# Kernel tuning notes

Measured on AMD Instinct MI355X. Metric: run time of the kernel, lower is better.

Reference implementation:

```python
import jax, jax.numpy as jnp
import numpy as np
import math

B, C, L_SEQ, PRED = 32, 21, 512, 96
D, H, DFF, NLAYERS = 512, 8, 2048, 3
E = D // H
PATCH_LEN, STRIDE, PAD = 16, 8, 8
PATCH_NUM = (L_SEQ - PATCH_LEN) // STRIDE + 2  # 64
MA = 25          # moving-average kernel of series_decomp
FACTOR = 1
TOP_K = int(FACTOR * math.log(PATCH_NUM))  # top-k delays in AutoCorrelation


def _pos_embedding(max_len, d_model):
    pos = np.arange(max_len, dtype=np.float32)[:, None]
    div = np.exp(np.arange(0, d_model, 2, dtype=np.float32) * -(math.log(10000.0) / d_model))
    pe = np.zeros((max_len, d_model), np.float32)
    pe[:, 0::2] = np.sin(pos * div)
    pe[:, 1::2] = np.cos(pos * div)
    return jnp.asarray(pe)

POS_EMB = _pos_embedding(PATCH_NUM, D)


def setup_inputs():
    key = jax.random.key(0)
    ks = iter(jax.random.split(key, 48))
    g = lambda shape, s=0.02: jax.random.normal(next(ks), shape, jnp.float32) * s
    inp = {"x_enc": jax.random.normal(next(ks), (B, L_SEQ, C), jnp.float32)}
    inp["w_val"] = g((PATCH_LEN, D))  # PatchEmbedding value_embedding (no bias)
    for tag in ("ac", "sa"):
        for nm in ("Wq", "Wk", "Wv", "Wo"):
            inp[nm + "_" + tag] = g((NLAYERS, D, D))
        for nm in ("bq", "bk", "bv", "bo"):
            inp[nm + "_" + tag] = g((NLAYERS, D))
    inp["Wf"] = g((NLAYERS, 2 * D, D))
    inp["bf"] = g((NLAYERS, D))
    inp["W1"] = g((NLAYERS, D, DFF))   # conv1 (1x1, no bias)
    inp["W2"] = g((NLAYERS, DFF, D))   # conv2 (1x1, no bias)
    inp["bn_g"] = jnp.ones((D,), jnp.float32)
    inp["bn_b"] = jnp.zeros((D,), jnp.float32)
    inp["W_head"] = g((D * PATCH_NUM, PRED))
    inp["b_head"] = g((PRED,))
    return inp


def _proj_heads(x, W, b):
    N, L, _ = x.shape
    return (x @ W + b).reshape(N, L, H, E)


def _auto_corr(x, Wq, bq, Wk, bk, Wv, bv, Wo, bo):
    # AutoCorrelation (training-mode time_delay_agg): FFT correlation + top-k roll aggregation
    N, L, _ = x.shape
    q = _proj_heads(x, Wq, bq)
    k = _proj_heads(x, Wk, bk)
    v = _proj_heads(x, Wv, bv)
    qf = jnp.fft.rfft(q.transpose(0, 2, 3, 1), axis=-1)   # [N,H,E,Lf]
    kf = jnp.fft.rfft(k.transpose(0, 2, 3, 1), axis=-1)
    corr = jnp.fft.irfft(qf * jnp.conj(kf), n=L, axis=-1)  # [N,H,E,L]
    vals = v.transpose(0, 2, 3, 1)                          # [N,H,E,L]
    mean_corr = corr.mean(axis=(1, 2))                      # [N,L]
    _, top_idx = jax.lax.top_k(mean_corr.mean(axis=0), TOP_K)  # delays shared across batch
    w = jax.nn.softmax(mean_corr[:, top_idx], axis=-1)      # [N,TOP_K]
    rolled = jax.vmap(lambda s: jnp.roll(vals, -s, axis=-1))(top_idx)  # [K,N,H,E,L]
    agg = jnp.einsum('knhel,nk->nhel', rolled, w)
    return agg.transpose(0, 3, 1, 2).reshape(N, L, D) @ Wo + bo


def _full_attn(x, Wq, bq, Wk, bk, Wv, bv, Wo, bo):
    N, L, _ = x.shape
    q = _proj_heads(x, Wq, bq)
    k = _proj_heads(x, Wk, bk)
    v = _proj_heads(x, Wv, bv)
    scores = jnp.einsum('blhe,bshe->bhls', q, k) / math.sqrt(E)
    out = jnp.einsum('bhls,bshe->blhe', jax.nn.softmax(scores, axis=-1), v)
    return out.reshape(N, L, D) @ Wo + bo


def _decomp(x):
    # series_decomp: residual after edge-replicated moving average (returns seasonal part)
    half = (MA - 1) // 2
    xp = jnp.concatenate([jnp.repeat(x[:, :1], half, axis=1), x,
                          jnp.repeat(x[:, -1:], half, axis=1)], axis=1)
    cs = jnp.cumsum(xp, axis=1)
    cs = jnp.concatenate([jnp.zeros_like(cs[:, :1]), cs], axis=1)
    mean = (cs[:, MA:] - cs[:, :-MA]) / MA
    return x - mean


def _forward(x_enc, w_val, Wq_ac, bq_ac, Wk_ac, bk_ac, Wv_ac, bv_ac, Wo_ac, bo_ac,
             Wq_sa, bq_sa, Wk_sa, bk_sa, Wv_sa, bv_sa, Wo_sa, bo_sa,
             Wf, bf, W1, W2, bn_g, bn_b, W_head, b_head):
    # instance normalization over time
    means = x_enc.mean(axis=1, keepdims=True)                 # [B,1,C]
    xc = x_enc - means
    stdev = jnp.sqrt(xc.var(axis=1, keepdims=True) + 1e-5)    # [B,1,C]
    xn = xc / stdev
    # patch embedding (channel independent): replication-pad end, unfold, linear + pos emb
    xp = xn.transpose(0, 2, 1)                                # [B,C,L]
    xp = jnp.concatenate([xp, jnp.repeat(xp[..., -1:], PAD, axis=-1)], axis=-1)
    idx = jnp.arange(PATCH_NUM)[:, None] * STRIDE + jnp.arange(PATCH_LEN)[None, :]
    patches = xp[..., idx]                                    # [B,C,P,patch_len]
    x = patches.reshape(B * C, PATCH_NUM, PATCH_LEN) @ w_val + POS_EMB  # [B*C,P,D]
    # hybrid encoder layers
    for l in range(NLAYERS):
        a = _auto_corr(x, Wq_ac[l], bq_ac[l], Wk_ac[l], bk_ac[l], Wv_ac[l], bv_ac[l], Wo_ac[l], bo_ac[l])
        s = _full_attn(x, Wq_sa[l], bq_sa[l], Wk_sa[l], bk_sa[l], Wv_sa[l], bv_sa[l], Wo_sa[l], bo_sa[l])
        fused = jnp.concatenate([a, s], axis=-1) @ Wf[l] + bf[l]
        x = _decomp(x + fused)
        y = jax.nn.relu(x @ W1[l]) @ W2[l]                    # 1x1 convs == pointwise linears
        x = _decomp(x + y)
    # final BatchNorm1d over d_model channels (batch statistics, affine)
    mu = x.mean(axis=(0, 1))
    var = x.var(axis=(0, 1))
    x = (x - mu) / jnp.sqrt(var + 1e-5) * bn_g + bn_b
    # head: [B*C,P,D] -> [B,C,D,P] -> flat (d-major) -> pred_len
    enc = x.reshape(B, C, PATCH_NUM, D).transpose(0, 1, 3, 2).reshape(B, C, D * PATCH_NUM)
    dec = (enc @ W_head + b_head).transpose(0, 2, 1)          # [B,PRED,C]
    return dec * stdev[:, 0][:, None, :] + means[:, 0][:, None, :]


def reference(x_enc, w_val, Wq_ac, bq_ac, Wk_ac, bk_ac, Wv_ac, bv_ac, Wo_ac, bo_ac,
              Wq_sa, bq_sa, Wk_sa, bk_sa, Wv_sa, bv_sa, Wo_sa, bo_sa,
              Wf, bf, W1, W2, bn_g, bn_b, W_head, b_head):
    return _forward(x_enc, w_val, Wq_ac, bq_ac, Wk_ac, bk_ac, Wv_ac, bv_ac, Wo_ac, bo_ac,
                    Wq_sa, bq_sa, Wk_sa, bk_sa, Wv_sa, bv_sa, Wo_sa, bo_sa,
                    Wf, bf, W1, W2, bn_g, bn_b, W_head, b_head)
```

## Files before the change

kernel.cpp:

```cpp
#include <hip/hip_runtime.h>
#include <math.h>


typedef unsigned short u16;
typedef short s16x8 __attribute__((ext_vector_type(8)));
typedef u16 u16x8 __attribute__((ext_vector_type(8)));
typedef float f32x4 __attribute__((ext_vector_type(4)));

#define MROWS 43008
#define NSEQ  672

__device__ __forceinline__ float bf2f(u16 b) {
  union { unsigned u; float f; } v; v.u = ((unsigned)b) << 16; return v.f;
}
__device__ __forceinline__ u16 f2bf(float f) {
  union { float f; unsigned u; } v; v.f = f;
  unsigned r = v.u + 0x7FFFu + ((v.u >> 16) & 1u);
  return (u16)(r >> 16);
}

__device__ __forceinline__ void gload16(const u16* g, u16* l) {
  __builtin_amdgcn_global_load_lds(
      (const __attribute__((address_space(1))) unsigned int*)g,
      (__attribute__((address_space(3))) unsigned int*)l, 16, 0, 0);
}

__global__ __launch_bounds__(256) void zero_out_kernel(float* __restrict__ o, int n) {
  int i = blockIdx.x * 256 + threadIdx.x;
  if (i < n) o[i] = 0.f;
}

__global__ __launch_bounds__(256) void transpose_cvt_b(
    const float* __restrict__ W, u16* __restrict__ Wt, int K, int N,
    long long sW, long long sT) {
  __shared__ float t[32][33];
  int z = blockIdx.z;
  W += (size_t)z * sW;
  Wt += (size_t)z * sT;
  int k0 = blockIdx.x * 32, n0 = blockIdx.y * 32;
  int tx = threadIdx.x, ty = threadIdx.y;
#pragma unroll
  for (int i = 0; i < 32; i += 8)
    t[ty + i][tx] = W[(size_t)(k0 + ty + i) * N + n0 + tx];
  __syncthreads();
#pragma unroll
  for (int i = 0; i < 32; i += 8)
    Wt[(size_t)(n0 + ty + i) * K + k0 + tx] = f2bf(t[tx][ty + i]);
}

__global__ __launch_bounds__(256) void transpose_cvt_sa(
    const float* __restrict__ Wq_sa, const float* __restrict__ Wk_sa,
    const float* __restrict__ Wv_sa, u16* __restrict__ dst) {
  __shared__ float t[32][33];
  int z = blockIdx.z;
  int l = z / 3, wi = z % 3;
  const float* srcs[3] = {Wq_sa, Wk_sa, Wv_sa};
  const float* W = srcs[wi] + (size_t)l * 262144;
  u16* out = dst + ((size_t)l * 3 + wi) * 262144;
  int k0 = blockIdx.x * 32, n0 = blockIdx.y * 32;
  int tx = threadIdx.x, ty = threadIdx.y;
#pragma unroll
  for (int i = 0; i < 32; i += 8)
    t[ty + i][tx] = W[(size_t)(k0 + ty + i) * 512 + n0 + tx];
  __syncthreads();
#pragma unroll
  for (int i = 0; i < 32; i += 8)
    out[(size_t)(n0 + ty + i) * 512 + k0 + tx] = f2bf(t[tx][ty + i]);
}

__global__ __launch_bounds__(256) void cvt_bf16_fifteen(
    const float* __restrict__ Wo_ac, const float* __restrict__ Wo_sa,
    const float* __restrict__ Wv_ac, const float* __restrict__ Wq_ac,
    const float* __restrict__ Wk_ac, u16* __restrict__ dst) {
  int z = blockIdx.z;
  int l = z / 5, s = z % 5;
  const float* bases[5] = {Wo_ac, Wo_sa, Wv_ac, Wq_ac, Wk_ac};
  const float* src = bases[s] + (size_t)l * 262144;
  u16* out = dst + ((size_t)l * 5 + s) * 262144;
  int i = blockIdx.x * 256 + threadIdx.x;
  if (i < 262144) out[i] = f2bf(src[i]);
}

__global__ __launch_bounds__(512) void boa_eff_kernel(
    const float* __restrict__ Wo_ac, const float* __restrict__ bo_ac,
    const float* __restrict__ bv_ac, float* __restrict__ out) {
  int l = blockIdx.x;
  int i = threadIdx.x;
  const float* Wo = Wo_ac + (size_t)l * 262144;
  float s = bo_ac[l * 512 + i];
  for (int k = 0; k < 512; k++) s += bv_ac[l * 512 + k] * Wo[(size_t)k * 512 + i];
  out[l * 512 + i] = s;
}

__global__ __launch_bounds__(512) void bias_combine(
    const float* __restrict__ WfW, const float* __restrict__ bfW,
    const float* __restrict__ boa_eff, const float* __restrict__ bo_sa,
    float* __restrict__ out) {
  int l = blockIdx.x;
  const float* Wf = WfW + (size_t)l * 524288;
  int n = threadIdx.x;
  float s = bfW[l * 512 + n];
  for (int i = 0; i < 512; i++) s += boa_eff[l * 512 + i] * Wf[(size_t)i * 512 + n];
  for (int i = 0; i < 512; i++) s += bo_sa[l * 512 + i] * Wf[(size_t)(512 + i) * 512 + n];
  out[l * 512 + n] = s;
}

__global__ __launch_bounds__(512, 4) void gemm128x256_p3(
    const u16* __restrict__ A1, const u16* __restrict__ A2, int lda, int ksplit,
    const u16* __restrict__ Bt, int ldb,
    const float* __restrict__ b0, const float* __restrict__ b1,
    const float* __restrict__ b2,
    u16* __restrict__ C, int ldc, int K, int relu, int nb) {
  __shared__ u16 smA[2][128 * 32];
  __shared__ u16 smB[2][256 * 32];
  int g = blockIdx.x;
  if ((gridDim.x & 7) == 0) g = (g & 7) * (gridDim.x >> 3) + (g >> 3);
  int m0 = (g / nb) * 128, n0 = (g % nb) * 256;
  int tid = threadIdx.x, lane = tid & 63, wid = tid >> 6;
  int wr = wid >> 2, wc = wid & 3;
  int m_in = lane & 15, kq = lane >> 4;
  int sr = tid >> 2;
  int gsl = (((tid & 3) ^ ((sr >> 1) & 3)) * 8);

  int offA[4], offB[4];
#pragma unroll
  for (int mf = 0; mf < 4; mf++) {
    int row = wr * 64 + mf * 16 + m_in;
    offA[mf] = row * 32 + ((kq ^ ((row >> 1) & 3)) * 8);
  }
#pragma unroll
  for (int nf = 0; nf < 4; nf++) {
    int row = wc * 64 + nf * 16 + m_in;
    offB[nf] = row * 32 + ((kq ^ ((row >> 1) & 3)) * 8);
  }
  f32x4 acc[4][4];
#pragma unroll
  for (int i = 0; i < 4; i++)
#pragma unroll
    for (int j = 0; j < 4; j++) acc[i][j] = (f32x4){0.f, 0.f, 0.f, 0.f};

  int nt = K >> 5;
  auto STAGE = [&](int b, int t) {
    int k0 = t * 32;
    const u16* Ap; int kk;
    if (k0 < ksplit) { Ap = A1; kk = k0; } else { Ap = A2; kk = k0 - ksplit; }
    gload16(&Ap[(size_t)(m0 + sr) * lda + kk + gsl], &smA[b][wid * 512]);
    gload16(&Bt[(size_t)(n0 + sr) * ldb + k0 + gsl], &smB[b][wid * 512]);
    gload16(&Bt[(size_t)(n0 + 128 + sr) * ldb + k0 + gsl],
            &smB[b][4096 + wid * 512]);
  };

  STAGE(0, 0);
  int cb = 0;
  for (int t = 0; t < nt; ++t) {
    int tn = t + 1 < nt ? t + 1 : t;
    STAGE(cb ^ 1, tn);
    asm volatile("s_waitcnt vmcnt(3)" ::: "memory");
    asm volatile("s_barrier" ::: "memory");
    const u16* la = &smA[cb][0];
    const u16* lb = &smB[cb][0];
    s16x8 a_[4], b_[4];
#pragma unroll
    for (int mf = 0; mf < 4; mf++) a_[mf] = *(const s16x8*)&la[offA[mf]];
#pragma unroll
    for (int nf = 0; nf < 4; nf++) b_[nf] = *(const s16x8*)&lb[offB[nf]];
    __builtin_amdgcn_s_setprio(1);
#pragma unroll
    for (int mf = 0; mf < 4; mf++)
#pragma unroll
      for (int nf = 0; nf < 4; nf++)
        acc[mf][nf] = __builtin_amdgcn_mfma_f32_16x16x32_bf16(
            a_[mf], b_[nf], acc[mf][nf], 0, 0, 0);
    __builtin_amdgcn_s_setprio(0);
    asm volatile("s_barrier" ::: "memory");
    cb ^= 1;
  }
  int r0 = m0 + wr * 64 + (kq << 2);
#pragma unroll
  for (int mf = 0; mf < 4; mf++) {
#pragma unroll
    for (int nf = 0; nf < 4; nf++) {
      int col = n0 + wc * 64 + nf * 16 + m_in;
      const float* bp = (col < 512) ? b0 : (col < 1024 ? b1 : b2);
      float bv = bp ? bp[col & 511] : 0.f;
#pragma unroll
      for (int r = 0; r < 4; r++) {
        float v = acc[mf][nf][r] + bv;
        if (relu) v = fmaxf(v, 0.f);
        C[(size_t)(r0 + mf * 16 + r) * ldc + col] = f2bf(v);
      }
    }
  }
}

__global__ __launch_bounds__(512, 4) void gemm128x256(
    const u16* __restrict__ A1, const u16* __restrict__ A2, int lda, int ksplit,
    const u16* __restrict__ Bt, int ldb,
    const float* __restrict__ b0, const float* __restrict__ b1,
    const float* __restrict__ b2,
    u16* __restrict__ C, int ldc, int K, int relu, int nb, int dmode) {
  __shared__ u16 shm[36864];
  int g = blockIdx.x;
  if ((gridDim.x & 7) == 0) g = (g & 7) * (gridDim.x >> 3) + (g >> 3);
  int m0 = (g / nb) * 128, n0 = (g % nb) * 256;
  int tid = threadIdx.x, lane = tid & 63, wid = tid >> 6;
  int wr = wid >> 2, wc = wid & 3;
  int m_in = lane & 15, kq = lane >> 4;
  int sr = tid >> 2;
  int gsl = (((tid & 3) ^ ((sr >> 1) & 3)) * 8);

  int offA[4], offB[4];
#pragma unroll
  for (int mf = 0; mf < 4; mf++) {
    int row = wr * 64 + mf * 16 + m_in;
    offA[mf] = row * 32 + ((kq ^ ((row >> 1) & 3)) * 8);
  }
#pragma unroll
  for (int nf = 0; nf < 4; nf++) {
    int row = wc * 64 + nf * 16 + m_in;
    offB[nf] = row * 32 + ((kq ^ ((row >> 1) & 3)) * 8);
  }
  f32x4 acc[4][4];
#pragma unroll
  for (int i = 0; i < 4; i++)
#pragma unroll
    for (int j = 0; j < 4; j++) acc[i][j] = (f32x4){0.f, 0.f, 0.f, 0.f};

  int nt = K >> 5;
  auto STAGE = [&](int b, int t) {
    int k0 = t * 32;
    const u16* Ap; int kk;
    if (k0 < ksplit) { Ap = A1; kk = k0; } else { Ap = A2; kk = k0 - ksplit; }
    gload16(&Ap[(size_t)(m0 + sr) * lda + kk + gsl], &shm[b * 4096 + wid * 512]);
    gload16(&Bt[(size_t)(n0 + sr) * ldb + k0 + gsl],
            &shm[12288 + b * 8192 + wid * 512]);
    gload16(&Bt[(size_t)(n0 + 128 + sr) * ldb + k0 + gsl],
            &shm[12288 + b * 8192 + 4096 + wid * 512]);
  };

  STAGE(0, 0);
  STAGE(1, 1 < nt ? 1 : nt - 1);
  int cb = 0;
  for (int t = 0; t < nt; ++t) {
    int pf = t + 2 < nt ? t + 2 : nt - 1;
    int pb = cb + 2 >= 3 ? cb - 1 : cb + 2;
    STAGE(pb, pf);
    asm volatile("s_waitcnt vmcnt(6)" ::: "memory");
    asm volatile("s_barrier" ::: "memory");
    const u16* la = &shm[cb * 4096];
    const u16* lb = &shm[12288 + cb * 8192];
    s16x8 a_[4], b_[4];
#pragma unroll
    for (int mf = 0; mf < 4; mf++) a_[mf] = *(const s16x8*)&la[offA[mf]];
#pragma unroll
    for (int nf = 0; nf < 4; nf++) b_[nf] = *(const s16x8*)&lb[offB[nf]];
    __builtin_amdgcn_s_setprio(1);
#pragma unroll
    for (int mf = 0; mf < 4; mf++)
#pragma unroll
      for (int nf = 0; nf < 4; nf++)
        acc[mf][nf] = __builtin_amdgcn_mfma_f32_16x16x32_bf16(
            a_[mf], b_[nf], acc[mf][nf], 0, 0, 0);
    __builtin_amdgcn_s_setprio(0);
    asm volatile("s_barrier" ::: "memory");
    cb = cb + 1 >= 3 ? 0 : cb + 1;
  }
  int r0 = m0 + wr * 64 + (kq << 2);
  if (dmode == 0) {
#pragma unroll
    for (int mf = 0; mf < 4; mf++) {
#pragma unroll
      for (int nf = 0; nf < 4; nf++) {
        int col = n0 + wc * 64 + nf * 16 + m_in;
        const float* bp = (col < 512) ? b0 : (col < 1024 ? b1 : b2);
        float bv = bp ? bp[col & 511] : 0.f;
#pragma unroll
        for (int r = 0; r < 4; r++) {
          float v = acc[mf][nf][r] + bv;
          if (relu) v = fmaxf(v, 0.f);
          C[(size_t)(r0 + mf * 16 + r) * ldc + col] = f2bf(v);
        }
      }
    }
  } else {
    asm volatile("s_waitcnt vmcnt(0)" ::: "memory");
    __syncthreads();
    u16* wscr = &shm[wid * 4352];
#pragma unroll
    for (int mf = 0; mf < 4; mf++) {
#pragma unroll
      for (int nf = 0; nf < 4; nf++) {
        int col = n0 + wc * 64 + nf * 16 + m_in;
        float bv = b0 ? b0[col & 511] : 0.f;
#pragma unroll
        for (int r = 0; r < 4; r++) {
          int row = r0 + mf * 16 + r;
          float xv = bf2f(C[(size_t)row * 512 + col]);
          wscr[(mf * 16 + (kq << 2) + r) * 68 + nf * 16 + m_in] =
              f2bf(xv + acc[mf][nf][r] + bv);
        }
      }
    }
    __syncthreads();
    int c = lane;
    int d = n0 + wc * 64 + c;
    int nseq = (m0 + wr * 64) >> 6;
    float v[64];
#pragma unroll
    for (int l = 0; l < 64; l++) v[l] = bf2f(wscr[l * 68 + c]);
    float s = 12.f * v[0];
#pragma unroll
    for (int t2 = 0; t2 <= 12; t2++) s += v[t2];
#pragma unroll
    for (int l = 0; l < 64; l++) {
      float out = v[l] - s * (1.f / 25.f);
      C[((size_t)nseq * 64 + l) * 512 + d] = f2bf(out);
      if (l < 63) {
        int add = l + 13; if (add > 63) add = 63;
        int sub = l - 12; if (sub < 0) sub = 0;
        s += v[add] - v[sub];
      }
    }
  }
}

__global__ __launch_bounds__(256) void gemm128p(
    const u16* __restrict__ A1, const u16* __restrict__ A2, int lda, int ksplit,
    const u16* __restrict__ Bt, int ldb,
    const float* __restrict__ b0, const float* __restrict__ b1,
    const float* __restrict__ b2,
    u16* __restrict__ C, int ldc, int K, int relu, int nb,
    long long syA, long long syB, long long syC) {
  __shared__ u16 sm[3][8192];
  int zy = blockIdx.y;
  A1 += (size_t)zy * syA;
  A2 += (size_t)zy * syA;
  Bt += (size_t)zy * syB;
  C  += (size_t)zy * syC;
  int g = blockIdx.x;
  if ((gridDim.x & 7) == 0) g = (g & 7) * (gridDim.x >> 3) + (g >> 3);
  int m0 = (g / nb) * 128, n0 = (g % nb) * 128;
  int tid = threadIdx.x, lane = tid & 63, w = tid >> 6;
  int wr = w >> 1, wc = w & 1;
  int srow = w * 16 + (lane >> 2);
  int scol = (((lane & 3) ^ ((lane >> 3) & 3)) * 8);
  int m_in = lane & 15;
  int sgrp = lane >> 4;
  int offA[4], offB[4];
#pragma unroll
  for (int mf = 0; mf < 4; mf++) {
    int row = wr * 64 + mf * 16 + m_in;
    offA[mf] = row * 32 + ((sgrp ^ ((row >> 1) & 3)) * 8);
  }
#pragma unroll
  for (int nf = 0; nf < 4; nf++) {
    int row = wc * 64 + nf * 16 + m_in;
    offB[nf] = 4096 + row * 32 + ((sgrp ^ ((row >> 1) & 3)) * 8);
  }
  f32x4 acc[4][4];
#pragma unroll
  for (int i = 0; i < 4; i++)
#pragma unroll
    for (int j = 0; j < 4; j++) acc[i][j] = (f32x4){0.f, 0.f, 0.f, 0.f};

  int nt = K >> 5;
  auto STAGE = [&](int b, int t) {
    int k0 = t * 32;
    const u16* Ab; int kk;
    if (k0 < ksplit) { Ab = A1; kk = k0; } else { Ab = A2; kk = k0 - ksplit; }
    u16* base = &sm[b][0];
    gload16(&Ab[(size_t)(m0 + srow) * lda + kk + scol],      base + w * 512);
    gload16(&Ab[(size_t)(m0 + 64 + srow) * lda + kk + scol], base + 2048 + w * 512);
    gload16(&Bt[(size_t)(n0 + srow) * ldb + k0 + scol],      base + 4096 + w * 512);
    gload16(&Bt[(size_t)(n0 + 64 + srow) * ldb + k0 + scol], base + 6144 + w * 512);
  };

  STAGE(0, 0);
  STAGE(1, 1 < nt ? 1 : nt - 1);
  int cb = 0;
  for (int t = 0; t < nt; ++t) {
    int pf = t + 2 < nt ? t + 2 : nt - 1;
    int pb = cb + 2 >= 3 ? cb - 1 : cb + 2;
    STAGE(pb, pf);
    asm volatile("s_waitcnt vmcnt(8)" ::: "memory");
    asm volatile("s_barrier" ::: "memory");
    const u16* lb = &sm[cb][0];
    s16x8 a_[4], b_[4];
#pragma unroll
    for (int mf = 0; mf < 4; mf++) a_[mf] = *(const s16x8*)&lb[offA[mf]];
#pragma unroll
    for (int nf = 0; nf < 4; nf++) b_[nf] = *(const s16x8*)&lb[offB[nf]];
    __builtin_amdgcn_s_setprio(1);
#pragma unroll
    for (int mf = 0; mf < 4; mf++)
#pragma unroll
      for (int nf = 0; nf < 4; nf++)
        acc[mf][nf] = __builtin_amdgcn_mfma_f32_16x16x32_bf16(
            a_[mf], b_[nf], acc[mf][nf], 0, 0, 0);
    __builtin_amdgcn_s_setprio(0);
    asm volatile("s_barrier" ::: "memory");
    cb = cb + 1 >= 3 ? 0 : cb + 1;
  }
  int r0 = m0 + wr * 64 + (sgrp << 2);
  int cl = lane & 15;
#pragma unroll
  for (int mf = 0; mf < 4; mf++) {
#pragma unroll
    for (int nf = 0; nf < 4; nf++) {
      int col = n0 + wc * 64 + nf * 16 + cl;
      const float* bp = (col < 512) ? b0 : (col < 1024 ? b1 : b2);
      float bv = bp ? bp[col & 511] : 0.f;
#pragma unroll
      for (int r = 0; r < 4; r++) {
        float v = acc[mf][nf][r] + bv;
        if (relu) v = fmaxf(v, 0.f);
        C[(size_t)(r0 + mf * 16 + r) * ldc + col] = f2bf(v);
      }
    }
  }
}

__global__ __launch_bounds__(256) void gram_mc_kernel(
    const u16* __restrict__ Q, int ldq, const u16* __restrict__ K, int ldk,
    float* __restrict__ MC) {
  __shared__ u16 lA[64][40];
  __shared__ u16 lB[64][40];
  __shared__ float red[64];
  int n = blockIdx.x;
  int tid = threadIdx.x, lane = tid & 63, w = tid >> 6;
  int sr = tid >> 2, scol = (tid & 3) * 8;
  if (tid < 64) red[tid] = 0.f;
  f32x4 acc[4];
#pragma unroll
  for (int i = 0; i < 4; i++) acc[i] = (f32x4){0.f, 0.f, 0.f, 0.f};
  size_t bq = (size_t)n * 64 * ldq;
  size_t bk = (size_t)n * 64 * ldk;
  for (int k0 = 0; k0 < 512; k0 += 32) {
    *(u16x8*)&lA[sr][scol] = *(const u16x8*)&Q[bq + (size_t)sr * ldq + k0 + scol];
    *(u16x8*)&lB[sr][scol] = *(const u16x8*)&K[bk + (size_t)sr * ldk + k0 + scol];
    __syncthreads();
    int ar = w * 16 + (lane & 15);
    int kk = (lane >> 4) * 8;
    s16x8 af = *(const s16x8*)&lA[ar][kk];
#pragma unroll
    for (int nb = 0; nb < 4; nb++) {
      s16x8 bfr = *(const s16x8*)&lB[nb * 16 + (lane & 15)][kk];
      acc[nb] = __builtin_amdgcn_mfma_f32_16x16x32_bf16(af, bfr, acc[nb], 0, 0, 0);
    }
    __syncthreads();
  }
  int row0 = w * 16 + ((lane >> 4) << 2);
  int cl = lane & 15;
#pragma unroll
  for (int nb = 0; nb < 4; nb++) {
    int col = nb * 16 + cl;
#pragma unroll
    for (int r = 0; r < 4; r++)
      atomicAdd(&red[(row0 + r - col) & 63], acc[nb][r]);
  }
  __syncthreads();
  if (tid < 64) MC[n * 64 + tid] = red[tid] * (1.f / 512.f);
}

__global__ __launch_bounds__(256) void instnorm_kernel(
    const float* __restrict__ xe, float* __restrict__ MEANS, float* __restrict__ STDEV) {
  int n = blockIdx.x;
  int b = n / 21, c = n % 21;
  int tid = threadIdx.x;
  float v0 = xe[((size_t)b * 512 + tid) * 21 + c];
  float v1 = xe[((size_t)b * 512 + tid + 256) * 21 + c];
  float s = v0 + v1, ss = v0 * v0 + v1 * v1;
  for (int o = 32; o; o >>= 1) { s += __shfl_down(s, o); ss += __shfl_down(ss, o); }
  __shared__ float rs[4], rss[4];
  if ((tid & 63) == 0) { rs[tid >> 6] = s; rss[tid >> 6] = ss; }
  __syncthreads();
  if (tid == 0) {
    s = rs[0] + rs[1] + rs[2] + rs[3];
    ss = rss[0] + rss[1] + rss[2] + rss[3];
    float mean = s * (1.f / 512.f);
    float var = ss * (1.f / 512.f) - mean * mean;
    MEANS[n] = mean;
    STDEV[n] = sqrtf(var + 1e-5f);
  }
}

__global__ __launch_bounds__(256) void pe_kernel(float* __restrict__ PE) {
  int i = blockIdx.x * 256 + threadIdx.x;
  int p = i >> 9, d = i & 511;
  int k = d >> 1;
  float freq = expf(-(float)(2 * k) * (9.210340371976184f / 512.f));
  float ang = (float)p * freq;
  PE[i] = (d & 1) ? cosf(ang) : sinf(ang);
}

__global__ __launch_bounds__(256) void patch_kernel(
    const float* __restrict__ xe, const float* __restrict__ wv,
    const float* __restrict__ PE, const float* __restrict__ MEANS,
    const float* __restrict__ STDEV, u16* __restrict__ X) {
  __shared__ float pw[16][512];
  __shared__ float pat[8][16];
  int bx = blockIdx.x;
  int n = bx >> 3, pb = bx & 7;
  int b = n / 21, c = n % 21;
  int tid = threadIdx.x;
  float mean = MEANS[n], inv = 1.f / STDEV[n];
  for (int i = tid; i < 8192; i += 256) pw[i >> 9][i & 511] = wv[i];
  if (tid < 128) {
    int pp = tid >> 4, j = tid & 15;
    int l = (pb * 8 + pp) * 8 + j;
    if (l > 511) l = 511;
    pat[pp][j] = (xe[((size_t)b * 512 + l) * 21 + c] - mean) * inv;
  }
  __syncthreads();
  for (int i = tid; i < 4096; i += 256) {
    int pp = i >> 9, d = i & 511;
    int p = pb * 8 + pp;
    float s = PE[p * 512 + d];
#pragma unroll
    for (int j = 0; j < 16; j++) s += pat[pp][j] * pw[j][d];
    X[((size_t)n * 64 + p) * 512 + d] = f2bf(s);
  }
}

__global__ __launch_bounds__(256) void topk_softw_kernel(
    const float* __restrict__ MC, int* __restrict__ TIDX, float* __restrict__ WSM) {
  __shared__ float g[256];
  __shared__ float gt[64];
  __shared__ int dly[4];
  int tid = threadIdx.x;
  int tau = tid & 63, part = tid >> 6;
  float s = 0.f;
  for (int n = part * 168; n < (part + 1) * 168; n++) s += MC[n * 64 + tau];
  g[tid] = s;
  __syncthreads();
  if (tid < 64) gt[tid] = g[tid] + g[64 + tid] + g[128 + tid] + g[192 + tid];
  __syncthreads();
  if (tid == 0) {
    for (int j = 0; j < 4; j++) {
      int best = 0; float bv = -1e30f;
      for (int t = 0; t < 64; t++) if (gt[t] > bv) { bv = gt[t]; best = t; }
      dly[j] = best;
      TIDX[j] = best;
      gt[best] = -1e30f;
    }
  }
  __syncthreads();
  for (int n = tid; n < 672; n += 256) {
    float v[4], mx = -1e30f;
#pragma unroll
    for (int j = 0; j < 4; j++) { v[j] = MC[n * 64 + dly[j]]; mx = fmaxf(mx, v[j]); }
    float ssum = 0.f;
#pragma unroll
    for (int j = 0; j < 4; j++) { v[j] = __expf(v[j] - mx); ssum += v[j]; }
    float inv = 1.f / ssum;
#pragma unroll
    for (int j = 0; j < 4; j++) WSM[n * 4 + j] = v[j] * inv;
  }
}

__global__ __launch_bounds__(256) void agg_kernel(
    const u16* __restrict__ V, int ldv, const float* __restrict__ WSM,
    const int* __restrict__ TIDX, u16* __restrict__ OUT, int ldo) {
  __shared__ u16 xs[64][512];
  __shared__ float w[4];
  __shared__ int dly[4];
  int n = blockIdx.x;
  int tid = threadIdx.x;
  if (tid < 4) { w[tid] = WSM[n * 4 + tid]; dly[tid] = TIDX[tid]; }
  for (int i = tid; i < 64 * 64; i += 256) {
    int l = i >> 6, seg = (i & 63) * 8;
    *(u16x8*)&xs[l][seg] = *(const u16x8*)&V[((size_t)n * 64 + l) * ldv + seg];
  }
  __syncthreads();
  for (int i = tid; i < 64 * 512; i += 256) {
    int l = i >> 9, d = i & 511;
    float s = 0.f;
#pragma unroll
    for (int j = 0; j < 4; j++)
      s += w[j] * bf2f(xs[(l + dly[j]) & 63][d]);
    OUT[((size_t)n * 64 + l) * ldo + d] = f2bf(s);
  }
}

__global__ __launch_bounds__(256) void attn_mfma(u16* __restrict__ QKV) {
  __shared__ u16 lq[64][72], lk[64][72], lvt[64][72], lp[64][72];
  int n = blockIdx.x >> 3, h = blockIdx.x & 7;
  size_t base = (size_t)n * 64 * 1536;
  int qo = h * 64, ko = 512 + h * 64, vo = 1024 + h * 64;
  int tid = threadIdx.x, lane = tid & 63, w = tid >> 6;
  int r = tid >> 2, c0 = (tid & 3) * 16;
  *(u16x8*)&lq[r][c0]     = *(const u16x8*)&QKV[base + (size_t)r * 1536 + qo + c0];
  *(u16x8*)&lq[r][c0 + 8] = *(const u16x8*)&QKV[base + (size_t)r * 1536 + qo + c0 + 8];
  *(u16x8*)&lk[r][c0]     = *(const u16x8*)&QKV[base + (size_t)r * 1536 + ko + c0];
  *(u16x8*)&lk[r][c0 + 8] = *(const u16x8*)&QKV[base + (size_t)r * 1536 + ko + c0 + 8];
  u16x8 v0 = *(const u16x8*)&QKV[base + (size_t)r * 1536 + vo + c0];
  u16x8 v1 = *(const u16x8*)&QKV[base + (size_t)r * 1536 + vo + c0 + 8];
#pragma unroll
  for (int j = 0; j < 8; j++) { lvt[c0 + j][r] = v0[j]; lvt[c0 + 8 + j][r] = v1[j]; }
  __syncthreads();
  int m_in = lane & 15, ks = (lane >> 4) * 8;
  int rq = lane >> 4;
  s16x8 aq0 = *(const s16x8*)&lq[w * 16 + m_in][ks];
  s16x8 aq1 = *(const s16x8*)&lq[w * 16 + m_in][32 + ks];
  f32x4 s4[4];
#pragma unroll
  for (int nf = 0; nf < 4; nf++) {
    s4[nf] = (f32x4){0.f, 0.f, 0.f, 0.f};
    s16x8 b0 = *(const s16x8*)&lk[nf * 16 + m_in][ks];
    s16x8 b1 = *(const s16x8*)&lk[nf * 16 + m_in][32 + ks];
    s4[nf] = __builtin_amdgcn_mfma_f32_16x16x32_bf16(aq0, b0, s4[nf], 0, 0, 0);
    s4[nf] = __builtin_amdgcn_mfma_f32_16x16x32_bf16(aq1, b1, s4[nf], 0, 0, 0);
  }
  float mx[4] = {-1e30f, -1e30f, -1e30f, -1e30f};
#pragma unroll
  for (int nf = 0; nf < 4; nf++)
#pragma unroll
    for (int r4 = 0; r4 < 4; r4++) {
      s4[nf][r4] *= 0.125f;
      mx[r4] = fmaxf(mx[r4], s4[nf][r4]);
    }
#pragma unroll
  for (int o = 1; o < 16; o <<= 1)
#pragma unroll
    for (int r4 = 0; r4 < 4; r4++) mx[r4] = fmaxf(mx[r4], __shfl_xor(mx[r4], o));
  float sum[4] = {0.f, 0.f, 0.f, 0.f};
#pragma unroll
  for (int nf = 0; nf < 4; nf++)
#pragma unroll
    for (int r4 = 0; r4 < 4; r4++) {
      float e = __expf(s4[nf][r4] - mx[r4]);
      s4[nf][r4] = e;
      sum[r4] += e;
    }
#pragma unroll
  for (int o = 1; o < 16; o <<= 1)
#pragma unroll
    for (int r4 = 0; r4 < 4; r4++) sum[r4] += __shfl_xor(sum[r4], o);
#pragma unroll
  for (int nf = 0; nf < 4; nf++)
#pragma unroll
    for (int r4 = 0; r4 < 4; r4++)
      lp[w * 16 + rq * 4 + r4][nf * 16 + m_in] = f2bf(s4[nf][r4] / sum[r4]);
  __syncthreads();
  s16x8 ap0 = *(const s16x8*)&lp[w * 16 + m_in][ks];
  s16x8 ap1 = *(const s16x8*)&lp[w * 16 + m_in][32 + ks];
#pragma unroll
  for (int nf = 0; nf < 4; nf++) {
    f32x4 o4 = (f32x4){0.f, 0.f, 0.f, 0.f};
    s16x8 b0 = *(const s16x8*)&lvt[nf * 16 + m_in][ks];
    s16x8 b1 = *(const s16x8*)&lvt[nf * 16 + m_in][32 + ks];
    o4 = __builtin_amdgcn_mfma_f32_16x16x32_bf16(ap0, b0, o4, 0, 0, 0);
    o4 = __builtin_amdgcn_mfma_f32_16x16x32_bf16(ap1, b1, o4, 0, 0, 0);
#pragma unroll
    for (int r4 = 0; r4 < 4; r4++)
      QKV[base + (size_t)(w * 16 + rq * 4 + r4) * 1536 + qo + nf * 16 + m_in] =
          f2bf(o4[r4]);
  }
}

__global__ __launch_bounds__(256) void bn_part(
    const u16* __restrict__ X, float* __restrict__ PS) {
  int ch = blockIdx.x, tid = threadIdx.x;
  float s1a = 0, s2a = 0, s1b = 0, s2b = 0;
  size_t base = (size_t)ch * 128 * 512;
  for (int r = 0; r < 128; r++) {
    float a = bf2f(X[base + (size_t)r * 512 + tid]);
    float b = bf2f(X[base + (size_t)r * 512 + tid + 256]);
    s1a += a; s2a += a * a; s1b += b; s2b += b * b;
  }
  PS[(size_t)(ch * 2 + 0) * 512 + tid] = s1a;
  PS[(size_t)(ch * 2 + 0) * 512 + tid + 256] = s1b;
  PS[(size_t)(ch * 2 + 1) * 512 + tid] = s2a;
  PS[(size_t)(ch * 2 + 1) * 512 + tid + 256] = s2b;
}

__global__ __launch_bounds__(256) void bn_final(
    const float* __restrict__ PS, const float* __restrict__ g,
    const float* __restrict__ b, float* __restrict__ SCALE, float* __restrict__ SHIFT) {
  int d = blockIdx.x * 256 + threadIdx.x;
  float s = 0, ss = 0;
  for (int c = 0; c < 336; c++) {
    s += PS[(size_t)(c * 2) * 512 + d];
    ss += PS[(size_t)(c * 2 + 1) * 512 + d];
  }
  float mu = s * (1.f / 43008.f);
  float var = ss * (1.f / 43008.f) - mu * mu;
  float inv = 1.f / sqrtf(var + 1e-5f);
  float sc = g[d] * inv;
  SCALE[d] = sc;
  SHIFT[d] = b[d] - mu * sc;
}

__global__ __launch_bounds__(256) void bn_transpose_kernel(
    const u16* __restrict__ X, const float* __restrict__ SCALE,
    const float* __restrict__ SHIFT, u16* __restrict__ ENC) {
  __shared__ u16 t[64][72];
  int n = blockIdx.x >> 3, dc = (blockIdx.x & 7) * 64;
  int tid = threadIdx.x;
  for (int i = tid; i < 4096; i += 256) {
    int p = i >> 6, d = i & 63;
    float v = bf2f(X[((size_t)n * 64 + p) * 512 + dc + d]) * SCALE[dc + d] + SHIFT[dc + d];
    t[p][d] = f2bf(v);
  }
  __syncthreads();
  for (int i = tid; i < 4096; i += 256) {
    int d = i >> 6, p = i & 63;
    ENC[(size_t)n * 32768 + (size_t)(dc + d) * 64 + p] = t[p][d];
  }
}

__global__ __launch_bounds__(256) void head_gemm(
    const u16* __restrict__ ENC, const u16* __restrict__ Wht,
    float* __restrict__ PART) {
  __shared__ u16 lA[64][40];
  __shared__ u16 lB[96][40];
  int bm = blockIdx.x;
  int kc = blockIdx.y;
  int tid = threadIdx.x, lane = tid & 63, w = tid >> 6;
  int sr = tid >> 2, sc0 = (tid & 3) * 8;
  f32x4 acc[6];
#pragma unroll
  for (int i = 0; i < 6; i++) acc[i] = (f32x4){0.f, 0.f, 0.f, 0.f};
  for (int kk0 = 0; kk0 < 1024; kk0 += 32) {
    int k0 = kc * 1024 + kk0;
    *(u16x8*)&lA[sr][sc0] =
        *(const u16x8*)&ENC[(size_t)(bm * 64 + sr) * 32768 + k0 + sc0];
    for (int i = tid; i < 96 * 4; i += 256) {
      int rB = i >> 2, seg = (i & 3) * 8;
      *(u16x8*)&lB[rB][seg] = *(const u16x8*)&Wht[(size_t)rB * 32768 + k0 + seg];
    }
    __syncthreads();
    int ar = w * 16 + (lane & 15);
    int kk = (lane >> 4) * 8;
    s16x8 af = *(const s16x8*)&lA[ar][kk];
#pragma unroll
    for (int nb = 0; nb < 6; nb++) {
      s16x8 bfr = *(const s16x8*)&lB[nb * 16 + (lane & 15)][kk];
      acc[nb] = __builtin_amdgcn_mfma_f32_16x16x32_bf16(af, bfr, acc[nb], 0, 0, 0);
    }
    __syncthreads();
  }
  int rb = bm * 64 + w * 16 + ((lane >> 4) << 2);
  int cl = lane & 15;
#pragma unroll
  for (int nb = 0; nb < 6; nb++) {
    int col = nb * 16 + cl;
#pragma unroll
    for (int r = 0; r < 4; r++) {
      int row = rb + r;
      if (row < 672) PART[((size_t)kc * 672 + row) * 96 + col] = acc[nb][r];
    }
  }
}

__global__ __launch_bounds__(256) void head_reduce(
    const float* __restrict__ PART, const float* __restrict__ bh,
    const float* __restrict__ STDEV, const float* __restrict__ MEANS,
    float* __restrict__ OUT) {
  int i = blockIdx.x * 256 + threadIdx.x;
  if (i >= 672 * 96) return;
  int n = i / 96, r = i % 96;
  float s = bh[r];
  for (int kc = 0; kc < 32; kc++) s += PART[((size_t)kc * 672 + n) * 96 + r];
  int b = n / 21, c = n % 21;
  OUT[((size_t)b * 96 + r) * 21 + c] = s * STDEV[n] + MEANS[n];
}

extern "C" void kernel_launch(void* const* d_in, const int* in_sizes, int n_in,
                              void* d_out, int out_size, void* d_ws, size_t ws_size,
                              hipStream_t stream) {
  const float* x_enc = (const float*)d_in[0];
  const float* w_val = (const float*)d_in[1];
  const float* Wq_ac = (const float*)d_in[2];
  const float* Wk_ac = (const float*)d_in[3];
  const float* Wv_ac = (const float*)d_in[4];
  const float* Wo_ac = (const float*)d_in[5];
  const float* bq_ac = (const float*)d_in[6];
  const float* bk_ac = (const float*)d_in[7];
  const float* bv_ac = (const float*)d_in[8];
  const float* bo_ac = (const float*)d_in[9];
  const float* Wq_sa = (const float*)d_in[10];
  const float* Wk_sa = (const float*)d_in[11];
  const float* Wv_sa = (const float*)d_in[12];
  const float* Wo_sa = (const float*)d_in[13];
  const float* bq_sa = (const float*)d_in[14];
  const float* bk_sa = (const float*)d_in[15];
  const float* bv_sa = (const float*)d_in[16];
  const float* bo_sa = (const float*)d_in[17];
  const float* WfW   = (const float*)d_in[18];
  const float* bfW   = (const float*)d_in[19];
  const float* W1    = (const float*)d_in[20];
  const float* W2    = (const float*)d_in[21];
  const float* bn_g  = (const float*)d_in[22];
  const float* bn_b  = (const float*)d_in[23];
  const float* W_head = (const float*)d_in[24];
  const float* b_head = (const float*)d_in[25];
  (void)in_sizes; (void)n_in; (void)out_size;
  (void)bq_ac; (void)bk_ac;

  char* wsp = (char*)d_ws;
  size_t off = 0;
  auto alloc = [&](size_t bytes) -> void* {
    void* p = wsp + off;
    off += (bytes + 255) & ~(size_t)255;
    return p;
  };
  u16* X    = (u16*)alloc((size_t)MROWS * 512 * 2);
  u16* Q3   = (u16*)alloc((size_t)MROWS * 1536 * 2);
  u16* SIX   = (u16*)alloc((size_t)3 * 3 * 262144 * 2);
  u16* W1T   = (u16*)alloc((size_t)3 * 1048576 * 2);
  u16* W2T   = (u16*)alloc((size_t)3 * 1048576 * 2);
  u16* WFT   = (u16*)alloc((size_t)3 * 524288 * 2);
  u16* WORIG = (u16*)alloc((size_t)3 * 5 * 262144 * 2);
  u16* WCOMB = (u16*)alloc((size_t)3 * 524288 * 2);
  u16* WQKT  = (u16*)alloc((size_t)3 * 262144 * 2);
  u16* WHT   = (u16*)alloc((size_t)3145728 * 2);
  u16* TMP   = (u16*)alloc((size_t)3 * 262144 * 2);
  float* PE = (float*)alloc((size_t)32768 * 4);
  float* MEANS = (float*)alloc(672 * 4);
  float* STDEV = (float*)alloc(672 * 4);
  float* MC = (float*)alloc(672 * 64 * 4);
  int* TIDX = (int*)alloc(4 * 4);
  float* WSM = (float*)alloc(672 * 4 * 4);
  float* BNP = (float*)alloc((size_t)336 * 1024 * 4);
  float* SCALE = (float*)alloc(512 * 4);
  float* SHIFT = (float*)alloc(512 * 4);
  float* BOAE = (float*)alloc(3 * 512 * 4);
  float* BCOMB = (float*)alloc(3 * 512 * 4);
  u16* C0 = Q3;
  u16* C1 = Q3 + 512;
  u16* C2 = Q3 + 1024;
  u16* HBUF = Q3;
  u16* ENC  = Q3;
  float* HEADP = (float*)X;

  if (off > ws_size) {
    zero_out_kernel<<<252, 256, 0, stream>>>((float*)d_out, 672 * 96);
    return;
  }

  transpose_cvt_sa<<<dim3(16, 16, 9), dim3(32, 8), 0, stream>>>(
      Wq_sa, Wk_sa, Wv_sa, SIX);
  transpose_cvt_b<<<dim3(16, 64, 3), dim3(32, 8), 0, stream>>>(
      W1, W1T, 512, 2048, 1048576, 1048576);
  transpose_cvt_b<<<dim3(64, 16, 3), dim3(32, 8), 0, stream>>>(
      W2, W2T, 2048, 512, 1048576, 1048576);
  transpose_cvt_b<<<dim3(32, 16, 3), dim3(32, 8), 0, stream>>>(
      WfW, WFT, 1024, 512, 524288, 524288);
  transpose_cvt_b<<<dim3(1024, 3, 1), dim3(32, 8), 0, stream>>>(
      W_head, WHT, 32768, 96, 0, 0);
  cvt_bf16_fifteen<<<dim3(1024, 1, 15), 256, 0, stream>>>(
      Wo_ac, Wo_sa, Wv_ac, Wq_ac, Wk_ac, WORIG);
  boa_eff_kernel<<<3, 512, 0, stream>>>(Wo_ac, bo_ac, bv_ac, BOAE);
  bias_combine<<<3, 512, 0, stream>>>(WfW, bfW, BOAE, bo_sa, BCOMB);
  gemm128p<<<dim3(16, 3), 256, 0, stream>>>(
      WFT, WFT, 1024, 512, WORIG, 512, nullptr, nullptr, nullptr,
      TMP, 512, 512, 0, 4, 524288, 5 * 262144, 262144);
  gemm128p<<<dim3(16, 3), 256, 0, stream>>>(
      TMP, TMP, 512, 512, WORIG + 2 * 262144, 512, nullptr, nullptr, nullptr,
      WCOMB, 1024, 512, 0, 4, 262144, 5 * 262144, 524288);
  gemm128p<<<dim3(16, 3), 256, 0, stream>>>(
      WFT + 512, WFT + 512, 1024, 512, WORIG + 262144, 512,
      nullptr, nullptr, nullptr, WCOMB + 512, 1024, 512, 0, 4,
      524288, 5 * 262144, 524288);
  gemm128p<<<dim3(16, 3), 256, 0, stream>>>(
      WORIG + 4 * 262144, WORIG + 4 * 262144, 512, 512,
      WORIG + 3 * 262144, 512, nullptr, nullptr, nullptr,
      WQKT, 512, 512, 0, 4, 5 * 262144, 5 * 262144, 262144);

  instnorm_kernel<<<672, 256, 0, stream>>>(x_enc, MEANS, STDEV);
  pe_kernel<<<128, 256, 0, stream>>>(PE);
  patch_kernel<<<672 * 8, 256, 0, stream>>>(x_enc, w_val, PE, MEANS, STDEV, X);

  auto gp3 = [&](const u16* A1, const u16* A2, int lda, int ksplit,
                 const u16* Bt, int ldb, const float* b0, const float* b1,
                 const float* b2, u16* C, int ldc, int M, int N, int K,
                 int relu) {
    int nb = N / 256;
    if (nb < 1) nb = 1;
    gemm128x256_p3<<<(M / 128) * nb, 512, 0, stream>>>(
        A1, A2, lda, ksplit, Bt, ldb, b0, b1, b2, C, ldc, K, relu, nb);
  };
  auto gbig = [&](const u16* A1, const u16* A2, int lda, int ksplit,
                  const u16* Bt, int ldb, const float* b0, const float* b1,
                  const float* b2, u16* C, int ldc, int M, int N, int K,
                  int relu, int dmode) {
    int nb = N / 256;
    if (nb < 1) nb = 1;
    gemm128x256<<<(M / 128) * nb, 512, 0, stream>>>(
        A1, A2, lda, ksplit, Bt, ldb, b0, b1, b2, C, ldc, K, relu, nb, dmode);
  };

  for (int l = 0; l < 3; l++) {
    const u16* qkv_sa = SIX + (size_t)l * 3 * 262144;
    const u16* wqkt   = WQKT + (size_t)l * 262144;
    const u16* w1     = W1T + (size_t)l * 1048576;
    const u16* w2     = W2T + (size_t)l * 1048576;
    const u16* wcomb  = WCOMB + (size_t)l * 524288;
    gp3(X, X, 512, 512, qkv_sa, 512, bq_sa + l * 512, bk_sa + l * 512,
        bv_sa + l * 512, Q3, 1536, MROWS, 1536, 512, 0);
    attn_mfma<<<5376, 256, 0, stream>>>(Q3);
    gp3(X, X, 512, 512, wqkt, 512, nullptr, nullptr, nullptr,
        C1, 1536, MROWS, 512, 512, 0);
    gram_mc_kernel<<<672, 256, 0, stream>>>(C1, 1536, X, 512, MC);
    topk_softw_kernel<<<1, 256, 0, stream>>>(MC, TIDX, WSM);
    agg_kernel<<<672, 256, 0, stream>>>(X, 512, WSM, TIDX, C2, 1536);
    gbig(C2, C0, 1536, 512, wcomb, 1024, BCOMB + l * 512, nullptr, nullptr,
         X, 512, MROWS, 512, 1024, 0, 1);
    for (int c = 0; c < 2; c++) {
      const u16* Xc = X + (size_t)c * 21504 * 512;
      u16* Xcw = X + (size_t)c * 21504 * 512;
      gp3(Xc, Xc, 512, 512, w1, 512, nullptr, nullptr, nullptr,
          HBUF, 2048, 21504, 2048, 512, 1);
      gbig(HBUF, HBUF, 2048, 2048, w2, 2048, nullptr, nullptr, nullptr,
           Xcw, 512, 21504, 512, 2048, 0, 1);
    }
  }

  bn_part<<<336, 256, 0, stream>>>(X, BNP);
  bn_final<<<2, 256, 0, stream>>>(BNP, bn_g, bn_b, SCALE, SHIFT);
  bn_transpose_kernel<<<672 * 8, 256, 0, stream>>>(X, SCALE, SHIFT, ENC);
  head_gemm<<<dim3(11, 32), 256, 0, stream>>>(ENC, WHT, HEADP);
  head_reduce<<<252, 256, 0, stream>>>(HEADP, b_head, STDEV, MEANS, (float*)d_out);
}
```

Baseline: 1.968 ms.

## Replace 128x256 GEMM with 256x256 tile, K=64 staged, interleaved load/MFMA pipeline

Replaces the 128x256 K=32 GEMM used for the QKV, Q·K-weight and FFN-up projections with a 256x256 tile kernel that stages K=64 per iteration. It uses an 8-way XOR swizzle and splits each K step into four MFMA phases interleaved with half-tile global-to-LDS loads. A and B are prefetched at different distances. The larger tile raises arithmetic intensity and cuts redundant global loads. The cost is doubled LDS use (64KB per block), more accumulator registers and lower occupancy (launch bound 2).

```diff
diff --git a/kernel.cpp b/kernel.cpp
--- a/kernel.cpp
+++ b/kernel.cpp
@@ -105,79 +105,131 @@
   out[l * 512 + n] = s;
 }
 
-__global__ __launch_bounds__(512, 4) void gemm128x256_p3(
+__global__ __launch_bounds__(512, 2) void gemm256q(
     const u16* __restrict__ A1, const u16* __restrict__ A2, int lda, int ksplit,
     const u16* __restrict__ Bt, int ldb,
     const float* __restrict__ b0, const float* __restrict__ b1,
     const float* __restrict__ b2,
     u16* __restrict__ C, int ldc, int K, int relu, int nb) {
-  __shared__ u16 smA[2][128 * 32];
-  __shared__ u16 smB[2][256 * 32];
+  __shared__ u16 smA[2][16384];
+  __shared__ u16 smB[2][16384];
   int g = blockIdx.x;
   if ((gridDim.x & 7) == 0) g = (g & 7) * (gridDim.x >> 3) + (g >> 3);
-  int m0 = (g / nb) * 128, n0 = (g % nb) * 256;
+  int m0 = (g / nb) * 256, n0 = (g % nb) * 256;
   int tid = threadIdx.x, lane = tid & 63, wid = tid >> 6;
   int wr = wid >> 2, wc = wid & 3;
   int m_in = lane & 15, kq = lane >> 4;
-  int sr = tid >> 2;
-  int gsl = (((tid & 3) ^ ((sr >> 1) & 3)) * 8);
-
-  int offA[4], offB[4];
-#pragma unroll
-  for (int mf = 0; mf < 4; mf++) {
-    int row = wr * 64 + mf * 16 + m_in;
-    offA[mf] = row * 32 + ((kq ^ ((row >> 1) & 3)) * 8);
+
+  int offA[8], offB[4];
+#pragma unroll
+  for (int mf = 0; mf < 8; mf++) {
+    int row = wr * 128 + mf * 16 + m_in;
+    offA[mf] = row * 64 + ((kq ^ (row & 7)) * 8);
   }
 #pragma unroll
   for (int nf = 0; nf < 4; nf++) {
     int row = wc * 64 + nf * 16 + m_in;
-    offB[nf] = row * 32 + ((kq ^ ((row >> 1) & 3)) * 8);
-  }
-  f32x4 acc[4][4];
-#pragma unroll
-  for (int i = 0; i < 4; i++)
+    offB[nf] = row * 64 + ((kq ^ (row & 7)) * 8);
+  }
+  int sr0 = tid >> 3;
+  int sc0 = (((tid & 7) ^ (sr0 & 7)) * 8);
+  int sd0 = tid * 8;
+
+  f32x4 acc[8][4];
+#pragma unroll
+  for (int i = 0; i < 8; i++)
 #pragma unroll
     for (int j = 0; j < 4; j++) acc[i][j] = (f32x4){0.f, 0.f, 0.f, 0.f};
 
-  int nt = K >> 5;
-  auto STAGE = [&](int b, int t) {
-    int k0 = t * 32;
-    const u16* Ap; int kk;
+  int nkt = K >> 6;
+  auto SA = [&](int db, int t2, int h) {
+    int k0 = t2 * 64; const u16* Ap; int kk;
     if (k0 < ksplit) { Ap = A1; kk = k0; } else { Ap = A2; kk = k0 - ksplit; }
-    gload16(&Ap[(size_t)(m0 + sr) * lda + kk + gsl], &smA[b][wid * 512]);
-    gload16(&Bt[(size_t)(n0 + sr) * ldb + k0 + gsl], &smB[b][wid * 512]);
-    gload16(&Bt[(size_t)(n0 + 128 + sr) * ldb + k0 + gsl],
-            &smB[b][4096 + wid * 512]);
+    const u16* base = Ap + (size_t)(m0 + h * 128) * lda + kk;
+    gload16(base + (size_t)sr0 * lda + sc0,        &smA[db][h * 8192 + sd0]);
+    gload16(base + (size_t)(64 + sr0) * lda + sc0, &smA[db][h * 8192 + 4096 + sd0]);
   };
-
-  STAGE(0, 0);
-  int cb = 0;
-  for (int t = 0; t < nt; ++t) {
-    int tn = t + 1 < nt ? t + 1 : t;
-    STAGE(cb ^ 1, tn);
-    asm volatile("s_waitcnt vmcnt(3)" ::: "memory");
-    asm volatile("s_barrier" ::: "memory");
-    const u16* la = &smA[cb][0];
-    const u16* lb = &smB[cb][0];
-    s16x8 a_[4], b_[4];
-#pragma unroll
-    for (int mf = 0; mf < 4; mf++) a_[mf] = *(const s16x8*)&la[offA[mf]];
-#pragma unroll
-    for (int nf = 0; nf < 4; nf++) b_[nf] = *(const s16x8*)&lb[offB[nf]];
+  auto SB = [&](int db, int t2, int h) {
+    int k0 = t2 * 64;
+    const u16* base = Bt + (size_t)(n0 + h * 128) * ldb + k0;
+    gload16(base + (size_t)sr0 * ldb + sc0,        &smB[db][h * 8192 + sd0]);
+    gload16(base + (size_t)(64 + sr0) * ldb + sc0, &smB[db][h * 8192 + 4096 + sd0]);
+  };
+
+  SA(0, 0, 0); SA(0, 0, 1);
+  SB(0, 0, 0); SB(0, 0, 1);
+  SA(1, 1, 0); SA(1, 1, 1);
+  asm volatile("s_waitcnt vmcnt(4)" ::: "memory");
+  asm volatile("s_barrier" ::: "memory");
+
+  for (int t = 0; t < nkt; ++t) {
+    int bb = t & 1;
+    const u16* la = &smA[bb][0];
+    const u16* lb = &smB[bb][0];
+    int tB = (t + 1 < nkt) ? t + 1 : t;
+    int tA = (t + 2 < nkt) ? t + 2 : t;
+    s16x8 a0[8], a1[8], b_[2][2];
+#pragma unroll
+    for (int mf = 0; mf < 8; mf++) a0[mf] = *(const s16x8*)&la[offA[mf]];
+    b_[0][0] = *(const s16x8*)&lb[offB[0]];
+    b_[1][0] = *(const s16x8*)&lb[offB[1]];
+    SB(bb ^ 1, tB, 0);
+    asm volatile("s_barrier" ::: "memory");
+    asm volatile("s_waitcnt lgkmcnt(0)" ::: "memory");
     __builtin_amdgcn_s_setprio(1);
 #pragma unroll
-    for (int mf = 0; mf < 4; mf++)
-#pragma unroll
-      for (int nf = 0; nf < 4; nf++)
-        acc[mf][nf] = __builtin_amdgcn_mfma_f32_16x16x32_bf16(
-            a_[mf], b_[nf], acc[mf][nf], 0, 0, 0);
+    for (int mf = 0; mf < 8; mf++) {
+      acc[mf][0] = __builtin_amdgcn_mfma_f32_16x16x32_bf16(a0[mf], b_[0][0], acc[mf][0], 0, 0, 0);
+      acc[mf][1] = __builtin_amdgcn_mfma_f32_16x16x32_bf16(a0[mf], b_[1][0], acc[mf][1], 0, 0, 0);
+    }
     __builtin_amdgcn_s_setprio(0);
     asm volatile("s_barrier" ::: "memory");
-    cb ^= 1;
-  }
-  int r0 = m0 + wr * 64 + (kq << 2);
-#pragma unroll
-  for (int mf = 0; mf < 4; mf++) {
+#pragma unroll
+    for (int mf = 0; mf < 8; mf++) a1[mf] = *(const s16x8*)&la[offA[mf] ^ 32];
+    b_[0][1] = *(const s16x8*)&lb[offB[0] ^ 32];
+    b_[1][1] = *(const s16x8*)&lb[offB[1] ^ 32];
+    SB(bb ^ 1, tB, 1);
+    asm volatile("s_barrier" ::: "memory");
+    asm volatile("s_waitcnt lgkmcnt(0)" ::: "memory");
+    __builtin_amdgcn_s_setprio(1);
+#pragma unroll
+    for (int mf = 0; mf < 8; mf++) {
+      acc[mf][0] = __builtin_amdgcn_mfma_f32_16x16x32_bf16(a1[mf], b_[0][1], acc[mf][0], 0, 0, 0);
+      acc[mf][1] = __builtin_amdgcn_mfma_f32_16x16x32_bf16(a1[mf], b_[1][1], acc[mf][1], 0, 0, 0);
+    }
+    __builtin_amdgcn_s_setprio(0);
+    asm volatile("s_barrier" ::: "memory");
+    b_[0][0] = *(const s16x8*)&lb[offB[2]];
+    b_[1][0] = *(const s16x8*)&lb[offB[3]];
+    SA(bb, tA, 0);
+    asm volatile("s_barrier" ::: "memory");
+    asm volatile("s_waitcnt lgkmcnt(0)" ::: "memory");
+    __builtin_amdgcn_s_setprio(1);
+#pragma unroll
+    for (int mf = 0; mf < 8; mf++) {
+      acc[mf][2] = __builtin_amdgcn_mfma_f32_16x16x32_bf16(a0[mf], b_[0][0], acc[mf][2], 0, 0, 0);
+      acc[mf][3] = __builtin_amdgcn_mfma_f32_16x16x32_bf16(a0[mf], b_[1][0], acc[mf][3], 0, 0, 0);
+    }
+    __builtin_amdgcn_s_setprio(0);
+    asm volatile("s_barrier" ::: "memory");
+    b_[0][1] = *(const s16x8*)&lb[offB[2] ^ 32];
+    b_[1][1] = *(const s16x8*)&lb[offB[3] ^ 32];
+    SA(bb, tA, 1);
+    asm volatile("s_waitcnt vmcnt(4)" ::: "memory");
+    asm volatile("s_barrier" ::: "memory");
+    asm volatile("s_waitcnt lgkmcnt(0)" ::: "memory");
+    __builtin_amdgcn_s_setprio(1);
+#pragma unroll
+    for (int mf = 0; mf < 8; mf++) {
+      acc[mf][2] = __builtin_amdgcn_mfma_f32_16x16x32_bf16(a1[mf], b_[0][1], acc[mf][2], 0, 0, 0);
+      acc[mf][3] = __builtin_amdgcn_mfma_f32_16x16x32_bf16(a1[mf], b_[1][1], acc[mf][3], 0, 0, 0);
+    }
+    __builtin_amdgcn_s_setprio(0);
+    asm volatile("s_barrier" ::: "memory");
+  }
+  int r0 = m0 + wr * 128 + (kq << 2);
+#pragma unroll
+  for (int mf = 0; mf < 8; mf++) {
 #pragma unroll
     for (int nf = 0; nf < 4; nf++) {
       int col = n0 + wc * 64 + nf * 16 + m_in;
@@ -872,13 +924,12 @@
   pe_kernel<<<128, 256, 0, stream>>>(PE);
   patch_kernel<<<672 * 8, 256, 0, stream>>>(x_enc, w_val, PE, MEANS, STDEV, X);
 
-  auto gp3 = [&](const u16* A1, const u16* A2, int lda, int ksplit,
-                 const u16* Bt, int ldb, const float* b0, const float* b1,
-                 const float* b2, u16* C, int ldc, int M, int N, int K,
-                 int relu) {
+  auto g256 = [&](const u16* A1, const u16* A2, int lda, int ksplit,
+                  const u16* Bt, int ldb, const float* b0, const float* b1,
+                  const float* b2, u16* C, int ldc, int M, int N, int K,
+                  int relu) {
     int nb = N / 256;
-    if (nb < 1) nb = 1;
-    gemm128x256_p3<<<(M / 128) * nb, 512, 0, stream>>>(
+    gemm256q<<<(M / 256) * nb, 512, 0, stream>>>(
         A1, A2, lda, ksplit, Bt, ldb, b0, b1, b2, C, ldc, K, relu, nb);
   };
   auto gbig = [&](const u16* A1, const u16* A2, int lda, int ksplit,
@@ -897,11 +948,11 @@
     const u16* w1     = W1T + (size_t)l * 1048576;
     const u16* w2     = W2T + (size_t)l * 1048576;
     const u16* wcomb  = WCOMB + (size_t)l * 524288;
-    gp3(X, X, 512, 512, qkv_sa, 512, bq_sa + l * 512, bk_sa + l * 512,
-        bv_sa + l * 512, Q3, 1536, MROWS, 1536, 512, 0);
+    g256(X, X, 512, 512, qkv_sa, 512, bq_sa + l * 512, bk_sa + l * 512,
+         bv_sa + l * 512, Q3, 1536, MROWS, 1536, 512, 0);
     attn_mfma<<<5376, 256, 0, stream>>>(Q3);
-    gp3(X, X, 512, 512, wqkt, 512, nullptr, nullptr, nullptr,
-        C1, 1536, MROWS, 512, 512, 0);
+    g256(X, X, 512, 512, wqkt, 512, nullptr, nullptr, nullptr,
+         C1, 1536, MROWS, 512, 512, 0);
     gram_mc_kernel<<<672, 256, 0, stream>>>(C1, 1536, X, 512, MC);
     topk_softw_kernel<<<1, 256, 0, stream>>>(MC, TIDX, WSM);
     agg_kernel<<<672, 256, 0, stream>>>(X, 512, WSM, TIDX, C2, 1536);
@@ -910,8 +961,8 @@
     for (int c = 0; c < 2; c++) {
       const u16* Xc = X + (size_t)c * 21504 * 512;
       u16* Xcw = X + (size_t)c * 21504 * 512;
-      gp3(Xc, Xc, 512, 512, w1, 512, nullptr, nullptr, nullptr,
-          HBUF, 2048, 21504, 2048, 512, 1);
+      g256(Xc, Xc, 512, 512, w1, 512, nullptr, nullptr, nullptr,
+           HBUF, 2048, 21504, 2048, 512, 1);
       gbig(HBUF, HBUF, 2048, 2048, w2, 2048, nullptr, nullptr, nullptr,
            Xcw, 512, 21504, 512, 2048, 0, 1);
     }
```

Measured after the change: 2.097 ms. +6.5%, slower.
